# Optimization experiments

Hardware: AMD Instinct MI355X
Metric: run time of the kernel (lower is better)

The kernel has to match this reference:

```python
import jax, jax.numpy as jnp
import numpy as np

K = 16  # number of neighbors (init kwarg k)
N_POINTS = 8_000_000
D_FEAT = 6


def setup_inputs() -> dict:
    key = jax.random.key(0)
    k1, k2, k3 = jax.random.split(key, 3)
    P = jax.random.normal(k1, (N_POINTS, D_FEAT), dtype=jnp.float32)
    W = jax.random.normal(k2, (3, 10), dtype=jnp.float32) * 0.1  # nn.Linear(10, 3) weight
    b = jax.random.normal(k3, (3,), dtype=jnp.float32) * 0.1     # nn.Linear(10, 3) bias
    i = 12345
    return {"P": P, "W": W, "b": b, "i": i}


def reference(P, W, b, i):
    # --- knn(i): note torch .topk defaults to largest=True, so this faithfully
    # selects the K points with the LARGEST distance to point i.
    pi = P[i, :3]                                   # [3]
    d = jnp.linalg.norm(P[:, :3] - pi, axis=1)      # [N] streaming distance pass
    _, idx = jax.lax.top_k(d, K)                    # [K]
    near = P[idx]                                   # [K, D]
    nloc = near[:, :3]                              # [K, 3]

    # --- rel_pos_enc, vectorized over all K neighbors (one tiny GEMM)
    diff = pi[None, :] - nloc                       # [K, 3]
    dist = jnp.linalg.norm(diff, axis=1, keepdims=True)  # [K, 1]
    feat = jnp.concatenate(
        [jnp.broadcast_to(pi, (K, 3)), nloc, diff, dist], axis=1
    )                                               # [K, 10]
    R = feat @ W.T + b                              # [K, 3]

    # --- forward: concat neighbor coords with encoding
    return jnp.concatenate([nloc, R], axis=1)       # [K, 6]
```

## Files before the change

### kernel.cpp

```cpp
#include <hip/hip_runtime.h>
#include <math.h>

#define KTOP 16
#define B1   512
#define T1   512
#define T2   512

typedef unsigned long long ull;

__device__ __forceinline__ ull pack_key(float d, unsigned idx) {
    return ((ull)__float_as_uint(d) << 32) | (ull)(0xFFFFFFFFu - idx);
}

__device__ __forceinline__ void insert_key(ull (&k)[KTOP], ull key) {
    ull t = key;
#pragma unroll
    for (int j = 0; j < KTOP; ++j) {
        const ull a = k[j];
        const bool c = (t > a);
        k[j] = c ? t : a;
        t    = c ? a : t;
    }
}

__device__ __forceinline__ float dist3(float x, float y, float z,
                                       float px, float py, float pz) {
#pragma clang fp contract(off)
    const float dx = x - px;
    const float dy = y - py;
    const float dz = z - pz;
    const float s  = (dx * dx + dy * dy) + dz * dz;
    return sqrtf(s);
}

__global__ __launch_bounds__(T1, 4) void pass1_topk(const float* __restrict__ P,
                                                    const int*   __restrict__ ipq,
                                                    int n,
                                                    ull* __restrict__ cand) {
    const int tid    = threadIdx.x;
    const int gid    = blockIdx.x * T1 + tid;
    const int stride = B1 * T1;

    const int i0 = ipq[0];
    const float pix = P[6 * i0 + 0];
    const float piy = P[6 * i0 + 1];
    const float piz = P[6 * i0 + 2];

    ull k[KTOP];
#pragma unroll
    for (int j = 0; j < KTOP; ++j) k[j] = 0ull;

    const float4* __restrict__ P4 = (const float4*)P;
    const int nQuad = n >> 2;

    for (int q = gid; q < nQuad; q += stride) {
        const float4 r0 = P4[6 * q + 0];
        const float4 r1 = P4[6 * q + 1];
        const float4 r2 = P4[6 * q + 2];
        const float4 r3 = P4[6 * q + 3];
        const float4 r4 = P4[6 * q + 4];
        const float4 r5 = P4[6 * q + 5];
        const float d0 = dist3(r0.x, r0.y, r0.z, pix, piy, piz);
        const float d1 = dist3(r1.z, r1.w, r2.x, pix, piy, piz);
        const float d2 = dist3(r3.x, r3.y, r3.z, pix, piy, piz);
        const float d3 = dist3(r4.z, r4.w, r5.x, pix, piy, piz);
        const ull k0 = pack_key(d0, (unsigned)(4 * q + 0));
        const ull k1 = pack_key(d1, (unsigned)(4 * q + 1));
        const ull k2 = pack_key(d2, (unsigned)(4 * q + 2));
        const ull k3 = pack_key(d3, (unsigned)(4 * q + 3));
        if (k0 > k[KTOP - 1]) insert_key(k, k0);
        if (k1 > k[KTOP - 1]) insert_key(k, k1);
        if (k2 > k[KTOP - 1]) insert_key(k, k2);
        if (k3 > k[KTOP - 1]) insert_key(k, k3);
    }
    for (int p = (nQuad << 2) + gid; p < n; p += stride) {
        const float d = dist3(P[6 * p], P[6 * p + 1], P[6 * p + 2], pix, piy, piz);
        const ull key = pack_key(d, (unsigned)p);
        if (key > k[KTOP - 1]) insert_key(k, key);
    }

    __shared__ ull s_w[T1 / 64];
    __shared__ ull s_best;
    const int lane = tid & 63;
    const int wid  = tid >> 6;

    for (int r = 0; r < KTOP; ++r) {
        const ull mk = k[0];
        ull rv = mk;
#pragma unroll
        for (int m = 32; m >= 1; m >>= 1) {
            const ull ov = __shfl_xor(rv, m);
            if (ov > rv) rv = ov;
        }
        if (lane == 0) s_w[wid] = rv;
        __syncthreads();
        if (tid == 0) {
            ull b = s_w[0];
            for (int w = 1; w < T1 / 64; ++w) if (s_w[w] > b) b = s_w[w];
            s_best = b;
            cand[blockIdx.x * KTOP + r] = b;
        }
        __syncthreads();
        if (mk == s_best) {
#pragma unroll
            for (int j = 0; j < KTOP - 1; ++j) k[j] = k[j + 1];
            k[KTOP - 1] = 0ull;
        }
    }
}

__global__ __launch_bounds__(T2, 1) void pass2_final(const float* __restrict__ P,
                                                     const int*   __restrict__ ipq,
                                                     const float* __restrict__ W,
                                                     const float* __restrict__ bvec,
                                                     const ull*   __restrict__ cand,
                                                     float* __restrict__ out) {
    __shared__ ull s_w[T2 / 64];
    __shared__ ull s_best;
    __shared__ ull s_final[KTOP];

    const int tid  = threadIdx.x;
    const int lane = tid & 63;
    const int wid  = tid >> 6;

    ull k[KTOP];
    const ull* __restrict__ my = cand + (size_t)tid * KTOP;
#pragma unroll
    for (int j = 0; j < KTOP; ++j) k[j] = my[j];

    for (int r = 0; r < KTOP; ++r) {
        const ull mk = k[0];
        ull rv = mk;
#pragma unroll
        for (int m = 32; m >= 1; m >>= 1) {
            const ull ov = __shfl_xor(rv, m);
            if (ov > rv) rv = ov;
        }
        if (lane == 0) s_w[wid] = rv;
        __syncthreads();
        if (tid == 0) {
            ull b = s_w[0];
            for (int w = 1; w < T2 / 64; ++w) if (s_w[w] > b) b = s_w[w];
            s_best = b;
            s_final[r] = b;
        }
        __syncthreads();
        if (mk == s_best) {
#pragma unroll
            for (int j = 0; j < KTOP - 1; ++j) k[j] = k[j + 1];
            k[KTOP - 1] = 0ull;
        }
    }
    __syncthreads();

    if (tid < KTOP) {
        const ull kk = s_final[tid];
        const float d = __uint_as_float((unsigned)(kk >> 32));
        const unsigned idx = 0xFFFFFFFFu - (unsigned)(kk & 0xFFFFFFFFull);
        const int   i0  = ipq[0];
        const float pix = P[6 * i0 + 0], piy = P[6 * i0 + 1], piz = P[6 * i0 + 2];
        const float nx  = P[6 * (size_t)idx + 0];
        const float ny  = P[6 * (size_t)idx + 1];
        const float nz  = P[6 * (size_t)idx + 2];
        float dx, dy, dz;
        {
#pragma clang fp contract(off)
            dx = pix - nx; dy = piy - ny; dz = piz - nz;
        }
        const float feat[10] = { pix, piy, piz, nx, ny, nz, dx, dy, dz, d };
        float R[3];
#pragma unroll
        for (int r = 0; r < 3; ++r) {
            float acc = bvec[r];
#pragma unroll
            for (int c = 0; c < 10; ++c) acc += feat[c] * W[r * 10 + c];
            R[r] = acc;
        }
        out[6 * tid + 0] = nx;   out[6 * tid + 1] = ny;   out[6 * tid + 2] = nz;
        out[6 * tid + 3] = R[0]; out[6 * tid + 4] = R[1]; out[6 * tid + 5] = R[2];
    }
}

extern "C" void kernel_launch(void* const* d_in, const int* in_sizes, int n_in,
                              void* d_out, int out_size, void* d_ws, size_t ws_size,
                              hipStream_t stream) {
    const float* P    = (const float*)d_in[0];
    const float* W    = (const float*)d_in[1];
    const float* bvec = (const float*)d_in[2];
    const int*   ipq  = (const int*)d_in[3];
    float*       out  = (float*)d_out;

    const int n = in_sizes[0] / 6;
    ull* cand = (ull*)d_ws;

    pass1_topk<<<B1, T1, 0, stream>>>(P, ipq, n, cand);
    pass2_final<<<1, T2, 0, stream>>>(P, ipq, W, bvec, cand, out);
}
```

Before: 291.7 us.

## Stage point tiles through LDS with coalesced float4 loads and register prefetch

Pass 1 now loads each 512-point tile as fully coalesced float4 rows into shared memory, with the next tile prefetched into registers, and each thread reads two points from LDS. This replaces the strided six-float4-per-thread global reads. The grid changes to 2048 blocks of 256 threads, and pass 2 becomes a 1024-thread kernel that merges 32K candidates with insertion before the reduction. The cost is two block barriers per tile and a longer final merge over four times as many candidates.

```diff
diff --git a/kernel.cpp b/kernel.cpp
--- a/kernel.cpp
+++ b/kernel.cpp
@@ -2,9 +2,12 @@
 #include <math.h>
 
 #define KTOP 16
-#define B1   512
-#define T1   512
-#define T2   512
+#define T1   256
+#define B1   2048
+#define PTS_PER_TILE 512
+#define F4_PER_TILE  768
+#define T2   1024
+#define NC2  (B1 * KTOP)
 
 typedef unsigned long long ull;
 
@@ -37,9 +40,9 @@
                                                     const int*   __restrict__ ipq,
                                                     int n,
                                                     ull* __restrict__ cand) {
-    const int tid    = threadIdx.x;
-    const int gid    = blockIdx.x * T1 + tid;
-    const int stride = B1 * T1;
+    __shared__ float4 tile_f4[F4_PER_TILE];
+
+    const int tid = threadIdx.x;
 
     const int i0 = ipq[0];
     const float pix = P[6 * i0 + 0];
@@ -51,29 +54,44 @@
     for (int j = 0; j < KTOP; ++j) k[j] = 0ull;
 
     const float4* __restrict__ P4 = (const float4*)P;
-    const int nQuad = n >> 2;
-
-    for (int q = gid; q < nQuad; q += stride) {
-        const float4 r0 = P4[6 * q + 0];
-        const float4 r1 = P4[6 * q + 1];
-        const float4 r2 = P4[6 * q + 2];
-        const float4 r3 = P4[6 * q + 3];
-        const float4 r4 = P4[6 * q + 4];
-        const float4 r5 = P4[6 * q + 5];
-        const float d0 = dist3(r0.x, r0.y, r0.z, pix, piy, piz);
-        const float d1 = dist3(r1.z, r1.w, r2.x, pix, piy, piz);
-        const float d2 = dist3(r3.x, r3.y, r3.z, pix, piy, piz);
-        const float d3 = dist3(r4.z, r4.w, r5.x, pix, piy, piz);
-        const ull k0 = pack_key(d0, (unsigned)(4 * q + 0));
-        const ull k1 = pack_key(d1, (unsigned)(4 * q + 1));
-        const ull k2 = pack_key(d2, (unsigned)(4 * q + 2));
-        const ull k3 = pack_key(d3, (unsigned)(4 * q + 3));
+    const int nTiles = n / PTS_PER_TILE;
+
+    int tile = blockIdx.x;
+    float4 r0, r1, r2;
+    if (tile < nTiles) {
+        const int b = tile * F4_PER_TILE + tid;
+        r0 = P4[b];
+        r1 = P4[b + T1];
+        r2 = P4[b + 2 * T1];
+    }
+
+    for (; tile < nTiles; tile += B1) {
+        __syncthreads();
+        tile_f4[tid]          = r0;
+        tile_f4[tid + T1]     = r1;
+        tile_f4[tid + 2 * T1] = r2;
+        const int next = tile + B1;
+        if (next < nTiles) {
+            const int b = next * F4_PER_TILE + tid;
+            r0 = P4[b];
+            r1 = P4[b + T1];
+            r2 = P4[b + 2 * T1];
+        }
+        __syncthreads();
+
+        const float* lp = (const float*)tile_f4 + 12 * tid;
+        const float x0 = lp[0], y0 = lp[1],  z0 = lp[2];
+        const float x1 = lp[6], y1 = lp[7],  z1 = lp[8];
+        const unsigned id0 = (unsigned)(tile * PTS_PER_TILE + 2 * tid);
+        const float d0 = dist3(x0, y0, z0, pix, piy, piz);
+        const float d1 = dist3(x1, y1, z1, pix, piy, piz);
+        const ull k0 = pack_key(d0, id0);
+        const ull k1 = pack_key(d1, id0 + 1);
         if (k0 > k[KTOP - 1]) insert_key(k, k0);
         if (k1 > k[KTOP - 1]) insert_key(k, k1);
-        if (k2 > k[KTOP - 1]) insert_key(k, k2);
-        if (k3 > k[KTOP - 1]) insert_key(k, k3);
-    }
-    for (int p = (nQuad << 2) + gid; p < n; p += stride) {
+    }
+
+    for (int p = nTiles * PTS_PER_TILE + blockIdx.x * T1 + tid; p < n; p += B1 * T1) {
         const float d = dist3(P[6 * p], P[6 * p + 1], P[6 * p + 2], pix, piy, piz);
         const ull key = pack_key(d, (unsigned)p);
         if (key > k[KTOP - 1]) insert_key(k, key);
@@ -124,9 +142,13 @@
     const int wid  = tid >> 6;
 
     ull k[KTOP];
-    const ull* __restrict__ my = cand + (size_t)tid * KTOP;
-#pragma unroll
-    for (int j = 0; j < KTOP; ++j) k[j] = my[j];
+#pragma unroll
+    for (int j = 0; j < KTOP; ++j) k[j] = 0ull;
+
+    for (int c = tid; c < NC2; c += T2) {
+        const ull key = cand[c];
+        if (key > k[KTOP - 1]) insert_key(k, key);
+    }
 
     for (int r = 0; r < KTOP; ++r) {
         const ull mk = k[0];
```

New measurement: 330.5 us. +13.3%, slower.
